# Kernel optimization log

Measured on AMD Instinct MI355X. Metric: run time of the kernel, lower is better.

## Reference

```python
import jax, jax.numpy as jnp
import numpy as np

B, T, C, H, N = 2, 1024, 2048, 32, 64
KVH = 8                       # GQA kv heads
KV = KVH * N                  # 512
REP = H // KVH                # 4
EPS = 1e-6
LORA = [96, 96, 64, 256, 64]  # xw, xa, xv, xg, xk lora dims


def rmsnorm(x, w, eps=EPS):
    xf = x.astype(jnp.float32)
    var = jnp.mean(xf * xf, axis=-1, keepdims=True)
    return (w * (xf * jax.lax.rsqrt(var + eps))).astype(x.dtype)


def rotate_half(x):
    x1, x2 = jnp.split(x, 2, axis=-1)
    return jnp.concatenate([-x2, x1], axis=-1)


def rwkv7_scan(r, w, k, v, a, b, state0):
    # r,w,k,v,a,b: [B,T,H,N]; state0: [B,H,N,N] (value x key)
    # per step: S = S*exp(w) + (S@a) b^T + v k^T ; o = S @ r
    def step(S, inp):
        r_t, w_t, k_t, v_t, a_t, b_t = inp  # each [B,H,N]
        sa = jnp.einsum('bhvk,bhk->bhv', S, a_t)
        S = (S * jnp.exp(w_t)[:, :, None, :]
             + sa[..., None] * b_t[:, :, None, :]
             + v_t[..., None] * k_t[:, :, None, :])
        o = jnp.einsum('bhvk,bhk->bhv', S, r_t)
        return S, o
    seqs = tuple(jnp.moveaxis(t, 1, 0) for t in (r, w, k, v, a, b))
    S, o = jax.lax.scan(step, state0, seqs)
    return jnp.moveaxis(o, 0, 1), S


def setup_inputs() -> dict:
    key = jax.random.key(0)
    ks = jax.random.split(key, 24)
    g = lambda i, shape, s=0.02: jax.random.normal(ks[i], shape, jnp.float32) * s
    # real rope cache, theta = 1e6, rotary_dim = N
    pos = jnp.arange(T, dtype=jnp.float32)
    inv = 1.0 / (1e6 ** (jnp.arange(0, N, 2, dtype=jnp.float32) / N))
    ang = pos[:, None] * inv[None, :]
    ang = jnp.concatenate([ang, ang], axis=-1)  # [T, N]
    cos = jnp.broadcast_to(jnp.cos(ang)[None], (B, T, N))
    sin = jnp.broadcast_to(jnp.sin(ang)[None], (B, T, N))
    return dict(
        x_in=jax.random.normal(ks[0], (B, T, C), jnp.float32),
        v_first=jax.random.normal(ks[1], (B, T, KVH, N), jnp.float32),
        k_first=jax.random.normal(ks[2], (B, T, KVH, N), jnp.float32),
        state=jnp.zeros((B, H, N, N), jnp.float32),
        calc_cos=cos, calc_sin=sin,
        ln1=jnp.ones((C,), jnp.float32), ln2=jnp.ones((C,), jnp.float32),
        ln_r=jnp.ones((N,), jnp.float32), ln_k=jnp.ones((N,), jnp.float32),
        wavgk1=g(3, (C, sum(LORA))),
        w0=g(4, (H * N,)), w2=g(5, (LORA[0], H * N)),
        a0=g(6, (H * N,)), a2=g(7, (LORA[1], H * N)),
        v0=g(8, (KV,)), v2=g(9, (LORA[2], KV)),
        k0=g(10, (KV,)), k2=g(11, (LORA[4], KV)),
        g2=g(12, (LORA[3], H * N)),
        r_k=g(13, (H, N)),
        RKV_W=g(14, (C, H * N + 2 * KV)),
        O_W=g(15, (H * N, C)),
        R_bias=g(16, (H * N,)), K_bias=g(17, (KV,)), V_bias=g(18, (KV,)),
    )


def _forward(x_in, v_first, k_first, state, calc_cos, calc_sin,
             ln1, ln2, ln_r, ln_k, wavgk1, w0, w2, a0, a2, v0, v2,
             k0, k2, g2, r_k, RKV_W, O_W, R_bias, K_bias, V_bias):
    x = rmsnorm(x_in, ln1)
    xw, xa, xv, xg, xk = jnp.split(x @ wavgk1, np.cumsum(LORA)[:-1].tolist(), axis=-1)
    r, k, v = jnp.split(x @ RKV_W, [H * N, H * N + KV], axis=-1)
    r = (r + R_bias).reshape(B, T, H, N)
    k = (k + K_bias).reshape(B, T, KVH, N)
    v = (v + V_bias).reshape(B, T, KVH, N)
    r = rmsnorm(r, ln_r)
    k = rmsnorm(k, ln_k)
    cos = calc_cos[:, :, None, :]
    sin = calc_sin[:, :, None, :]
    r = r * cos + rotate_half(r) * sin
    k = k * cos + rotate_half(k) * sin
    # layer_id != 0: sigmoid-gated interpolation toward first-layer v/k
    v = v + (v_first - v) * jax.nn.sigmoid(xv @ v2 + v0).reshape(B, T, KVH, N)
    k = k + (k_first - k) * jax.nn.sigmoid(xk @ k2 + k0).reshape(B, T, KVH, N)
    # GQA repeat (contiguous per kv head, as repeat_kv does)
    k = jnp.repeat(k, REP, axis=2).reshape(B, T, H * N)
    v = jnp.repeat(v, REP, axis=2).reshape(B, T, H * N)
    a = jax.nn.sigmoid(xa @ a2 + a0)
    kh = k.reshape(B, T, H, N)
    kk = (kh / (jnp.linalg.norm(kh, axis=-1, keepdims=True) + 1e-12)).reshape(B, T, H * N)
    w = jnp.tanh(xw) @ w2 + w0
    w = -jax.nn.softplus(-w) - 0.5
    k = k * (1.0 - w + a)
    aa = -kk
    bb = kk * a
    wlog = -jnp.exp(w)
    sh = (B, T, H, N)
    o, state = rwkv7_scan(r, wlog.reshape(sh), k.reshape(sh), v.reshape(sh),
                          aa.reshape(sh), bb.reshape(sh), state)
    xx = o.reshape(B, T, H * N) * (float(N) ** -0.5)
    bonus = ((r * k.reshape(sh) * r_k).sum(axis=-1, keepdims=True)
             * v.reshape(sh)).reshape(B, T, H * N)
    xx = xx + bonus
    out = (xx * (jax.nn.sigmoid(xg) @ g2)) @ O_W
    x_res = x_in + out
    output = rmsnorm(x_res, ln2)
    return output, x[:, -1], state, v_first, k_first, x_res


def reference(x_in, v_first, k_first, state, calc_cos, calc_sin,
              ln1, ln2, ln_r, ln_k, wavgk1, w0, w2, a0, a2, v0, v2,
              k0, k2, g2, r_k, RKV_W, O_W, R_bias, K_bias, V_bias):
    return _forward(x_in, v_first, k_first, state, calc_cos, calc_sin,
                    ln1, ln2, ln_r, ln_k, wavgk1, w0, w2, a0, a2, v0, v2,
                    k0, k2, g2, r_k, RKV_W, O_W, R_bias, K_bias, V_bias)
```

## Files before the change

kernel.cpp:

```cpp
#include <hip/hip_runtime.h>
#include <hip/hip_bf16.h>

#define BT 2
#define TT 1024
#define CC 2048
#define HH 32
#define MM (BT*TT)
#define TCH 512
#define NCH (TT/TCH)
#define RECB 896

typedef __attribute__((ext_vector_type(8))) short short8;
typedef __attribute__((ext_vector_type(4))) float floatx4;

static __device__ __forceinline__ float bf2f(__hip_bfloat16 x){ return __bfloat162float(x); }
static __device__ __forceinline__ __hip_bfloat16 f2bf(float x){ return __float2bfloat16(x); }
static __device__ __forceinline__ float sigm(float x){ return 1.0f/(1.0f + expf(-x)); }
static __device__ __forceinline__ float u2f(unsigned short u){
  union { unsigned int i; float f; } x; x.i = ((unsigned int)u) << 16; return x.f;
}
static __device__ __forceinline__ float ulo(unsigned int u){ return __uint_as_float(u << 16); }
static __device__ __forceinline__ float uhi(unsigned int u){ return __uint_as_float(u & 0xffff0000u); }
static __device__ __forceinline__ unsigned short bfbits(float x){
  __hip_bfloat16 h = f2bf(x);
  unsigned short s; __builtin_memcpy(&s, &h, 2); return s;
}
static __device__ __forceinline__ unsigned int pkbf(float lo, float hi){
  return (unsigned int)bfbits(lo) | ((unsigned int)bfbits(hi) << 16);
}

#define DPP_ADD(x, ctrl) ((x) + __int_as_float(__builtin_amdgcn_update_dpp(0, __float_as_int(x), (ctrl), 0xF, 0xF, true)))

#if defined(__has_builtin)
#if __has_builtin(__builtin_amdgcn_permlane16_swap) && __has_builtin(__builtin_amdgcn_permlane32_swap)
#define HAVE_PLSWAP 1
#endif
#endif

#ifdef HAVE_PLSWAP
typedef unsigned int uint2v __attribute__((ext_vector_type(2)));
static __device__ __forceinline__ float row16_pair_add(float x){
  unsigned int u = __float_as_uint(x);
  uint2v r = __builtin_amdgcn_permlane16_swap(u, u, false, false);
  return __uint_as_float(r[0]) + __uint_as_float(r[1]);
}
static __device__ __forceinline__ float half32_pair_add(float x){
  unsigned int u = __float_as_uint(x);
  uint2v r = __builtin_amdgcn_permlane32_swap(u, u, false, false);
  return __uint_as_float(r[0]) + __uint_as_float(r[1]);
}
#else
static __device__ __forceinline__ float row16_pair_add(float x){ return x + __shfl_xor(x, 16); }
static __device__ __forceinline__ float half32_pair_add(float x){ return x + __shfl_xor(x, 32); }
#endif

static __device__ __forceinline__ float red8(float x){
  x = DPP_ADD(x, 0xB1);
  x = DPP_ADD(x, 0x4E);
  x = DPP_ADD(x, 0x141);
  return x;
}
static __device__ __forceinline__ float red32(float x){
  x = DPP_ADD(x, 0xB1);
  x = DPP_ADD(x, 0x4E);
  x = DPP_ADD(x, 0x124);
  x = DPP_ADD(x, 0x128);
  return row16_pair_add(x);
}
static __device__ __forceinline__ float red64(float x){
  x = DPP_ADD(x, 0xB1);
  x = DPP_ADD(x, 0x4E);
  x = DPP_ADD(x, 0x124);
  x = DPP_ADD(x, 0x128);
  x = row16_pair_add(x);
  return half32_pair_add(x);
}

__global__ __launch_bounds__(256) void tcvt_kernel(
    const float* __restrict__ W, __hip_bfloat16* __restrict__ Wt,
    int K, int N, int Npad)
{
  __shared__ float tile[32][33];
  const int bn = blockIdx.x*32, bk = blockIdx.y*32;
  const int tx = threadIdx.x & 31, ty0 = threadIdx.x >> 5;
#pragma unroll
  for (int i=0;i<4;++i){
    const int kk = bk + ty0 + i*8;
    float val = 0.f;
    if (kk < K && bn + tx < N) val = W[(size_t)kk*N + bn + tx];
    tile[ty0 + i*8][tx] = val;
  }
  __syncthreads();
#pragma unroll
  for (int i=0;i<4;++i){
    const int nn = bn + ty0 + i*8;
    const int kk = bk + tx;
    if (nn < Npad && kk < K) Wt[(size_t)nn*K + kk] = f2bf(tile[tx][ty0 + i*8]);
  }
}

__global__ __launch_bounds__(256) void rmsnorm1_kernel(
    const float* __restrict__ x_in,
    const float* __restrict__ ln1,
    __hip_bfloat16* __restrict__ x_bf,
    float* __restrict__ x_last)
{
  const int m = blockIdx.x;
  const int tid = threadIdx.x;
  const int c = tid * 8;
  const float* xp = x_in + (size_t)m*CC + c;
  float v[8]; float ss = 0.f;
#pragma unroll
  for (int i=0;i<8;++i){ v[i] = xp[i]; ss += v[i]*v[i]; }
  ss = red64(ss);
  __shared__ float wsum[4];
  if ((tid&63)==0) wsum[tid>>6] = ss;
  __syncthreads();
  ss = wsum[0]+wsum[1]+wsum[2]+wsum[3];
  const float sc = rsqrtf(ss * (1.0f/CC) + 1e-6f);
#pragma unroll
  for (int i=0;i<8;++i) {
    const float y = ln1[c+i] * v[i] * sc;
    x_bf[(size_t)m*CC + c + i] = f2bf(y);
    if ((m % TT) == TT-1) x_last[(size_t)(m/TT)*CC + c + i] = y;
  }
}

template<bool F32OUT>
__global__ __launch_bounds__(256) void mgemm(
    const __hip_bfloat16* __restrict__ A, int lda,
    const __hip_bfloat16* __restrict__ Bt,
    void* __restrict__ C, int N, int K)
{
  __shared__ __align__(16) short As[128*32];
  __shared__ __align__(16) short Bs[128*32];
  const int tid = threadIdx.x;
  const int bm = blockIdx.x * 128;
  const int bn = blockIdx.y * 128;
  const int wid = tid >> 6;
  const int lane = tid & 63;
  const int m16 = lane & 15, quad = lane >> 4;
  const int wm = wid & 1, wn = wid >> 1;
  const int lrow = tid >> 2;
  const int lcol = (tid & 3) * 8;

  floatx4 acc[4][4];
#pragma unroll
  for (int i=0;i<4;++i)
#pragma unroll
    for (int j=0;j<4;++j) acc[i][j] = (floatx4){0.f,0.f,0.f,0.f};

  for (int k0 = 0; k0 < K; k0 += 32) {
    __syncthreads();
    uint4 a0v = *(const uint4*)(const void*)(A  + (size_t)(bm + lrow)      * lda + k0 + lcol);
    uint4 a1v = *(const uint4*)(const void*)(A  + (size_t)(bm + 64 + lrow) * lda + k0 + lcol);
    uint4 b0v = *(const uint4*)(const void*)(Bt + (size_t)(bn + lrow)      * K   + k0 + lcol);
    uint4 b1v = *(const uint4*)(const void*)(Bt + (size_t)(bn + 64 + lrow) * K   + k0 + lcol);
    *(uint4*)(void*)(As + lrow*32 + lcol)        = a0v;
    *(uint4*)(void*)(As + (64 + lrow)*32 + lcol) = a1v;
    *(uint4*)(void*)(Bs + lrow*32 + lcol)        = b0v;
    *(uint4*)(void*)(Bs + (64 + lrow)*32 + lcol) = b1v;
    __syncthreads();

    short8 af[4], bfg[4];
#pragma unroll
    for (int mi=0; mi<4; ++mi)
      af[mi] = *(const short8*)(const void*)(As + (wm*64 + mi*16 + m16)*32 + quad*8);
#pragma unroll
    for (int ni=0; ni<4; ++ni)
      bfg[ni] = *(const short8*)(const void*)(Bs + (wn*64 + ni*16 + m16)*32 + quad*8);
#pragma unroll
    for (int mi=0; mi<4; ++mi)
#pragma unroll
      for (int ni=0; ni<4; ++ni)
        acc[mi][ni] = __builtin_amdgcn_mfma_f32_16x16x32_bf16(af[mi], bfg[ni], acc[mi][ni], 0,0,0);
  }

#pragma unroll
  for (int mi=0; mi<4; ++mi) {
    const int row = bm + wm*64 + mi*16 + quad*4;
#pragma unroll
    for (int ni=0; ni<4; ++ni) {
      const int col = bn + wn*64 + ni*16 + m16;
      if (col < N) {
        if (F32OUT) {
          float* cp = (float*)C;
#pragma unroll
          for (int r=0;r<4;++r) cp[(size_t)(row+r)*N + col] = acc[mi][ni][r];
        } else {
          __hip_bfloat16* cp = (__hip_bfloat16*)C;
#pragma unroll
          for (int r=0;r<4;++r) cp[(size_t)(row+r)*N + col] = f2bf(acc[mi][ni][r]);
        }
      }
    }
  }
}

__global__ void act576_kernel(__hip_bfloat16* __restrict__ Y1)
{
  int i = blockIdx.x*256 + threadIdx.x;
  if (i >= MM*576) return;
  int col = i % 576;
  float v = bf2f(Y1[i]);
  if (col < 96) v = tanhf(v);
  else if (col >= 256 && col < 512) v = sigm(v);
  Y1[i] = f2bf(v);
}

__global__ __launch_bounds__(256) void prep_kernel(
    const __hip_bfloat16* __restrict__ RKV,
    const __hip_bfloat16* __restrict__ Wpre,
    const __hip_bfloat16* __restrict__ Apre,
    const __hip_bfloat16* __restrict__ Vsig,
    const __hip_bfloat16* __restrict__ Ksig,
    const float* __restrict__ v_first,
    const float* __restrict__ k_first,
    const float* __restrict__ cosp,
    const float* __restrict__ sinp,
    const float* __restrict__ ln_r,
    const float* __restrict__ ln_k,
    const float* __restrict__ r_k,
    const float* __restrict__ w0,
    const float* __restrict__ a0,
    const float* __restrict__ v0,
    const float* __restrict__ k0b,
    const float* __restrict__ R_bias,
    const float* __restrict__ K_bias,
    const float* __restrict__ V_bias,
    char* __restrict__ rec,
    float* __restrict__ bonus,
    int t0)
{
  const int b    = blockIdx.x / TCH;
  const int tloc = blockIdx.x % TCH;
  const int t    = t0 + tloc;
  const int m    = b*TT + t;
  const int tid = threadIdx.x;
  const int h  = tid >> 3;
  const int j  = tid & 7;
  const int hk = h >> 2;
  const int nb = j * 8;
  const int hn = h*64 + nb;
  const int kn = hk*64 + nb;

  const size_t rbase = (size_t)m*3072 + h*64 + nb;
  const size_t kbase = (size_t)m*3072 + 2048 + kn;
  const size_t vbase = kbase + 512;

  float r[8], k[8], v[8];
  float ssr = 0.f, ssk = 0.f;
#pragma unroll
  for (int i=0;i<8;++i) {
    r[i] = bf2f(RKV[rbase+i]) + R_bias[hn+i];
    k[i] = bf2f(RKV[kbase+i]) + K_bias[kn+i];
    v[i] = bf2f(RKV[vbase+i]) + V_bias[kn+i];
    ssr += r[i]*r[i];
    ssk += k[i]*k[i];
  }
  ssr = red8(ssr);
  ssk = red8(ssk);
  const float scr = rsqrtf(ssr*(1.0f/64.0f) + 1e-6f);
  const float sck = rsqrtf(ssk*(1.0f/64.0f) + 1e-6f);
#pragma unroll
  for (int i=0;i<8;++i) {
    r[i] = ln_r[nb+i] * r[i] * scr;
    k[i] = ln_k[nb+i] * k[i] * sck;
  }
  const float sgn = (j < 4) ? -1.0f : 1.0f;
  float rr[8], kr[8];
#pragma unroll
  for (int i=0;i<8;++i) {
    const float cs = cosp[(size_t)m*64 + nb + i];
    const float sn = sinp[(size_t)m*64 + nb + i];
    const float pr = __shfl_xor(r[i], 4);
    const float pk = __shfl_xor(k[i], 4);
    rr[i] = r[i]*cs + sgn*pr*sn;
    kr[i] = k[i]*cs + sgn*pk*sn;
  }
  float av[8], ew[8], wv2[8];
  float ssn = 0.f;
#pragma unroll
  for (int i=0;i<8;++i) {
    const float vs = sigm(bf2f(Vsig[(size_t)m*512 + kn + i]) + v0[kn+i]);
    v[i]  = v[i]  + (v_first[(size_t)m*512 + kn + i] - v[i])  * vs;
    const float ks = sigm(bf2f(Ksig[(size_t)m*512 + kn + i]) + k0b[kn+i]);
    kr[i] = kr[i] + (k_first[(size_t)m*512 + kn + i] - kr[i]) * ks;
    ssn += kr[i]*kr[i];
    av[i] = sigm(bf2f(Apre[(size_t)m*2048 + hn + i]) + a0[hn+i]);
    float wraw = bf2f(Wpre[(size_t)m*2048 + hn + i]) + w0[hn+i];
    const float xs = -wraw;
    const float sp = fmaxf(xs, 0.f) + log1pf(expf(-fabsf(xs)));
    const float wv = -sp - 0.5f;
    wv2[i] = wv;
    ew[i] = expf(-expf(wv));
  }
  ssn = red8(ssn);
  const float inrm = 1.0f / (sqrtf(ssn) + 1e-12f);
  float kf[8], kkv[8];
  float bsum = 0.f;
#pragma unroll
  for (int i=0;i<8;++i) {
    kkv[i] = kr[i] * inrm;
    kf[i]  = kr[i] * (1.0f - wv2[i] + av[i]);
    bsum  += rr[i] * kf[i] * r_k[hn+i];
  }
  bsum = red8(bsum);

  char* base = rec + ((size_t)(b*HH + h)*TCH + tloc)*RECB;
  const int klb = nb >> 1;
#pragma unroll
  for (int p=0;p<4;++p) {
    const int i0 = 2*p, i1 = i0 + 1;
    uint4 Aw;
    Aw.x = __float_as_uint(ew[i0]);
    Aw.y = __float_as_uint(ew[i1]);
    Aw.z = pkbf(rr[i0], rr[i1]);
    Aw.w = pkbf(kf[i0], kf[i1]);
    *(uint4*)(void*)(base + (size_t)(klb + p)*16) = Aw;
    uint2 Bw;
    Bw.x = pkbf(kkv[i0], kkv[i1]);
    Bw.y = pkbf(-kkv[i0]*av[i0], -kkv[i1]*av[i1]);
    *(uint2*)(void*)(base + 512 + (size_t)(klb + p)*8) = Bw;
  }
  short8 vs8;
#pragma unroll
  for (int i=0;i<8;++i) vs8[i] = (short)bfbits(v[i]);
  *(short8*)(void*)(base + 768 + (size_t)nb*2) = vs8;
#pragma unroll
  for (int i=0;i<8;++i)
    bonus[(size_t)m*2048 + hn + i] = bsum * v[i];
}

__global__ __launch_bounds__(256) void scan_kernel(
    const char* __restrict__ rec,
    float* __restrict__ state,
    float* __restrict__ o_out,
    int t0)
{
  const int blk = blockIdx.x;
  const int bh  = blk & 63;
  const int q   = blk >> 6;
  const int b   = bh >> 5, h = bh & 31;
  const int tid = threadIdx.x;
  const int vl  = q*8 + (tid >> 5);
  const int kl  = tid & 31;
  const int k2  = kl*2;

  const char* base = rec + (size_t)bh * TCH * RECB;
  float* sp = state + ((size_t)bh*64 + vl)*64 + k2;
  float S0=sp[0], S1=sp[1];

  const char* pA = base + kl*16;
  const char* pB = base + 512 + kl*8;
  const char* pv = base + 768 + vl*2;

  uint4 Ab[4]; uint2 Bb[4]; unsigned short vb[4];
#pragma unroll
  for (int s=0;s<4;++s){
    Ab[s] = *(const uint4*)(const void*)(pA + s*RECB);
    Bb[s] = *(const uint2*)(const void*)(pB + s*RECB);
    vb[s] = *(const unsigned short*)(const void*)(pv + s*RECB);
  }
  pA += 4*RECB; pB += 4*RECB; pv += 4*RECB;

  int oidx = (b*TT + t0)*CC + h*64 + vl - CC;
  int tt = 0;
  float opart = 0.f;

#define SCAN_STEP(jj, PF)                                                      \
  {                                                                            \
    const uint4 A  = Ab[jj];                                                   \
    const uint2 Bv = Bb[jj];                                                   \
    const float vf = u2f(vb[jj]);                                              \
    if (PF) {                                                                  \
      Ab[jj] = *(const uint4*)(const void*)(pA + jj*RECB);                     \
      Bb[jj] = *(const uint2*)(const void*)(pB + jj*RECB);                     \
      vb[jj] = *(const unsigned short*)(const void*)(pv + jj*RECB);            \
    }                                                                          \
    float op = red32(opart);                                                   \
    const float kk0 = ulo(Bv.x), kk1 = uhi(Bv.x);                              \
    float sa = S0*kk0 + S1*kk1;                                                \
    sa = red32(sa);                                                            \
    if (kl == 0 && tt > 0) o_out[oidx] = op;                                   \
    S0 = S0*__uint_as_float(A.x) + sa*ulo(Bv.y) + vf*ulo(A.w);                 \
    S1 = S1*__uint_as_float(A.y) + sa*uhi(Bv.y) + vf*uhi(A.w);                 \
    opart = S0*ulo(A.z) + S1*uhi(A.z);                                         \
    ++tt; oidx += CC;                                                          \
  }

  for (int t = 0; t < TCH-4; t += 4) {
    SCAN_STEP(0, true)
    SCAN_STEP(1, true)
    SCAN_STEP(2, true)
    SCAN_STEP(3, true)
    pA += 4*RECB; pB += 4*RECB; pv += 4*RECB;
  }
  SCAN_STEP(0, false)
  SCAN_STEP(1, false)
  SCAN_STEP(2, false)
  SCAN_STEP(3, false)
#undef SCAN_STEP

  opart = red32(opart);
  if (kl == 0)
    o_out[oidx] = opart;

  sp[0]=S0; sp[1]=S1;
}

__global__ void xxg_kernel(const float* __restrict__ o_in,
                           const float* __restrict__ bonus,
                           const __hip_bfloat16* __restrict__ G,
                           __hip_bfloat16* __restrict__ xxg)
{
  int i = blockIdx.x*256 + threadIdx.x;
  xxg[i] = f2bf((o_in[i]*0.125f + bonus[i]) * bf2f(G[i]));
}

__global__ __launch_bounds__(256) void final_kernel(
    const float* __restrict__ x_in,
    const float* __restrict__ OUTb,
    const float* __restrict__ ln2,
    float* __restrict__ seg0,
    float* __restrict__ seg5)
{
  const int m = blockIdx.x;
  const int tid = threadIdx.x;
  const int c = tid*8;
  const float* xp = x_in + (size_t)m*CC + c;
  const float* op = OUTb + (size_t)m*CC + c;
  float xr[8]; float ss = 0.f;
#pragma unroll
  for (int i=0;i<8;++i){ xr[i] = xp[i] + op[i]; ss += xr[i]*xr[i]; }
#pragma unroll
  for (int i=0;i<8;++i) seg5[(size_t)m*CC + c + i] = xr[i];
  ss = red64(ss);
  __shared__ float wsum[4];
  if ((tid&63)==0) wsum[tid>>6] = ss;
  __syncthreads();
  ss = wsum[0]+wsum[1]+wsum[2]+wsum[3];
  const float sc = rsqrtf(ss*(1.0f/CC) + 1e-6f);
#pragma unroll
  for (int i=0;i<8;++i) seg0[(size_t)m*CC + c + i] = ln2[c+i] * xr[i] * sc;
}

extern "C" void kernel_launch(void* const* d_in, const int* in_sizes, int n_in,
                              void* d_out, int out_size, void* d_ws, size_t ws_size,
                              hipStream_t stream)
{
  (void)in_sizes; (void)n_in; (void)out_size; (void)ws_size;
  const float* x_in   = (const float*)d_in[0];
  const float* v_first= (const float*)d_in[1];
  const float* k_first= (const float*)d_in[2];
  const float* state0 = (const float*)d_in[3];
  const float* cosp   = (const float*)d_in[4];
  const float* sinp   = (const float*)d_in[5];
  const float* ln1    = (const float*)d_in[6];
  const float* ln2    = (const float*)d_in[7];
  const float* ln_r   = (const float*)d_in[8];
  const float* ln_k   = (const float*)d_in[9];
  const float* wavgk1 = (const float*)d_in[10];
  const float* w0     = (const float*)d_in[11];
  const float* w2     = (const float*)d_in[12];
  const float* a0     = (const float*)d_in[13];
  const float* a2     = (const float*)d_in[14];
  const float* v0     = (const float*)d_in[15];
  const float* v2     = (const float*)d_in[16];
  const float* k0b    = (const float*)d_in[17];
  const float* k2     = (const float*)d_in[18];
  const float* g2     = (const float*)d_in[19];
  const float* r_k    = (const float*)d_in[20];
  const float* RKV_W  = (const float*)d_in[21];
  const float* O_W    = (const float*)d_in[22];
  const float* R_bias = (const float*)d_in[23];
  const float* K_bias = (const float*)d_in[24];
  const float* V_bias = (const float*)d_in[25];

  float* out  = (float*)d_out;
  float* seg0 = out;
  float* seg1 = out + 4194304;
  float* seg2 = out + 4198400;
  float* seg3 = out + 4460544;
  float* seg4 = out + 5509120;
  float* seg5 = out + 6557696;

  char* ws = (char*)d_ws;
  const size_t OFF_STF   = 0;
  const size_t OFF_OWT   = 1048576;
  const size_t OFF_G     = 9437184;
  const size_t OFF_VSIG  = 17825792;
  const size_t OFF_KSIG  = 19922944;
  const size_t OFF_WPRE  = 22020096;
  const size_t OFF_APRE  = 30408704;
  const size_t OFF_RKV   = 38797312;
  const size_t OFF_XBF   = 51380224;
  const size_t OFF_Y1    = 59768832;
  const size_t OFF_WT    = 62128128;
  const size_t OFF_WAVT  = OFF_WT;
  const size_t OFF_RKVT  = OFF_WAVT + 2621440;
  const size_t OFF_W2T   = OFF_RKVT + 12582912;
  const size_t OFF_A2T   = OFF_W2T  + 393216;
  const size_t OFF_V2T   = OFF_A2T  + 393216;
  const size_t OFF_K2T   = OFF_V2T  + 65536;
  const size_t OFF_G2T   = OFF_K2T  + 65536;
  const size_t OFF_REC   = OFF_WT;
  const size_t OFF_XXG   = OFF_XBF;
  const size_t OFF_OUT   = OFF_WPRE;

  float*          stf   = (float*)(ws + OFF_STF);
  __hip_bfloat16* owt   = (__hip_bfloat16*)(ws + OFF_OWT);
  __hip_bfloat16* Gbuf  = (__hip_bfloat16*)(ws + OFF_G);
  __hip_bfloat16* Vsig  = (__hip_bfloat16*)(ws + OFF_VSIG);
  __hip_bfloat16* Ksig  = (__hip_bfloat16*)(ws + OFF_KSIG);
  __hip_bfloat16* Wpre  = (__hip_bfloat16*)(ws + OFF_WPRE);
  __hip_bfloat16* Apre  = (__hip_bfloat16*)(ws + OFF_APRE);
  __hip_bfloat16* RKV   = (__hip_bfloat16*)(ws + OFF_RKV);
  __hip_bfloat16* x_bf  = (__hip_bfloat16*)(ws + OFF_XBF);
  __hip_bfloat16* Y1    = (__hip_bfloat16*)(ws + OFF_Y1);
  __hip_bfloat16* wavt  = (__hip_bfloat16*)(ws + OFF_WAVT);
  __hip_bfloat16* rkvt  = (__hip_bfloat16*)(ws + OFF_RKVT);
  __hip_bfloat16* w2t   = (__hip_bfloat16*)(ws + OFF_W2T);
  __hip_bfloat16* a2t   = (__hip_bfloat16*)(ws + OFF_A2T);
  __hip_bfloat16* v2t   = (__hip_bfloat16*)(ws + OFF_V2T);
  __hip_bfloat16* k2t   = (__hip_bfloat16*)(ws + OFF_K2T);
  __hip_bfloat16* g2t   = (__hip_bfloat16*)(ws + OFF_G2T);
  char*           rec   = ws + OFF_REC;
  __hip_bfloat16* xxg   = (__hip_bfloat16*)(ws + OFF_XXG);
  float*          OUTb  = (float*)(ws + OFF_OUT);

  float* o_st = seg0;
  float* b_st = seg5;

  tcvt_kernel<<<dim3(20, 64), 256, 0, stream>>>(wavgk1, wavt, 2048, 576, 640);
  tcvt_kernel<<<dim3(96, 64), 256, 0, stream>>>(RKV_W,  rkvt, 2048, 3072, 3072);
  tcvt_kernel<<<dim3(64, 64), 256, 0, stream>>>(O_W,    owt,  2048, 2048, 2048);
  tcvt_kernel<<<dim3(64,  3), 256, 0, stream>>>(w2,     w2t,    96, 2048, 2048);
  tcvt_kernel<<<dim3(64,  3), 256, 0, stream>>>(a2,     a2t,    96, 2048, 2048);
  tcvt_kernel<<<dim3(16,  2), 256, 0, stream>>>(v2,     v2t,    64,  512,  512);
  tcvt_kernel<<<dim3(16,  2), 256, 0, stream>>>(k2,     k2t,    64,  512,  512);
  tcvt_kernel<<<dim3(64,  8), 256, 0, stream>>>(g2,     g2t,   256, 2048, 2048);

  rmsnorm1_kernel<<<MM, 256, 0, stream>>>(x_in, ln1, x_bf, seg1);
  mgemm<false><<<dim3(16,  5), 256, 0, stream>>>(x_bf, CC, wavt, Y1,   576, 2048);
  mgemm<false><<<dim3(16, 24), 256, 0, stream>>>(x_bf, CC, rkvt, RKV, 3072, 2048);
  act576_kernel<<<(MM*576+255)/256, 256, 0, stream>>>(Y1);
  mgemm<false><<<dim3(16, 16), 256, 0, stream>>>(Y1+0,   576, w2t, Wpre, 2048, 96);
  mgemm<false><<<dim3(16, 16), 256, 0, stream>>>(Y1+96,  576, a2t, Apre, 2048, 96);
  mgemm<false><<<dim3(16,  4), 256, 0, stream>>>(Y1+192, 576, v2t, Vsig,  512, 64);
  mgemm<false><<<dim3(16,  4), 256, 0, stream>>>(Y1+512, 576, k2t, Ksig,  512, 64);
  mgemm<false><<<dim3(16, 16), 256, 0, stream>>>(Y1+256, 576, g2t, Gbuf, 2048, 256);

  hipMemcpyAsync(stf, state0, (size_t)1048576, hipMemcpyDeviceToDevice, stream);
  for (int c = 0; c < NCH; ++c) {
    const int t0 = c*TCH;
    prep_kernel<<<BT*TCH, 256, 0, stream>>>(RKV, Wpre, Apre, Vsig, Ksig, v_first, k_first,
                                            cosp, sinp, ln_r, ln_k, r_k, w0, a0, v0, k0b,
                                            R_bias, K_bias, V_bias, rec, b_st, t0);
    scan_kernel<<<BT*HH*8, 256, 0, stream>>>(rec, stf, o_st, t0);
  }
  hipMemcpyAsync(seg2, stf, (size_t)1048576, hipMemcpyDeviceToDevice, stream);

  xxg_kernel<<<(MM*CC)/256, 256, 0, stream>>>(o_st, b_st, Gbuf, xxg);
  mgemm<true><<<dim3(16, 16), 256, 0, stream>>>(xxg, CC, owt, OUTb, 2048, 2048);
  final_kernel<<<MM, 256, 0, stream>>>(x_in, OUTb, ln2, seg0, seg5);

  hipMemcpyAsync(seg3, v_first, (size_t)1048576*4, hipMemcpyDeviceToDevice, stream);
  hipMemcpyAsync(seg4, k_first, (size_t)1048576*4, hipMemcpyDeviceToDevice, stream);
}
```

Before: 658.8 us.

## Use direct global-to-LDS loads in GEMM, fuse activation, pack scan math

The GEMM tile loads now go straight from global memory into LDS through the global_load_lds builtin when it is available, skipping the pass through registers. The tanh/sigmoid activation is moved into the epilogue of the first LoRA GEMM, which removes the separate act576 kernel and its extra read and write of Y1. The scan kernel's state update is rewritten with two-wide float vectors so the compiler can emit packed FP32 ops. Its first unrolled group is peeled, which drops the per-step check that skipped the output store on the first step. Risks are that the direct-to-LDS path depends on the compiler treating the per-lane LDS address as wave base plus lane offset, and that the packed math may not change the scan's serial latency.

```diff
diff --git a/kernel.cpp b/kernel.cpp
--- a/kernel.cpp
+++ b/kernel.cpp
@@ -12,6 +12,7 @@
 
 typedef __attribute__((ext_vector_type(8))) short short8;
 typedef __attribute__((ext_vector_type(4))) float floatx4;
+typedef __attribute__((ext_vector_type(2))) float f32x2;
 
 static __device__ __forceinline__ float bf2f(__hip_bfloat16 x){ return __bfloat162float(x); }
 static __device__ __forceinline__ __hip_bfloat16 f2bf(float x){ return __float2bfloat16(x); }
@@ -28,6 +29,21 @@
 static __device__ __forceinline__ unsigned int pkbf(float lo, float hi){
   return (unsigned int)bfbits(lo) | ((unsigned int)bfbits(hi) << 16);
 }
+
+#if defined(__has_builtin)
+#if __has_builtin(__builtin_amdgcn_global_load_lds)
+#define HAVE_GLL 1
+#endif
+#endif
+
+#ifdef HAVE_GLL
+static __device__ __forceinline__ void gll16(const void* g, void* l){
+  __builtin_amdgcn_global_load_lds(
+      (__attribute__((address_space(1))) void*)const_cast<void*>(g),
+      (__attribute__((address_space(3))) void*)l,
+      16, 0, 0);
+}
+#endif
 
 #define DPP_ADD(x, ctrl) ((x) + __int_as_float(__builtin_amdgcn_update_dpp(0, __float_as_int(x), (ctrl), 0xF, 0xF, true)))
 
@@ -126,7 +142,7 @@
   }
 }
 
-template<bool F32OUT>
+template<bool F32OUT, int ACT>
 __global__ __launch_bounds__(256) void mgemm(
     const __hip_bfloat16* __restrict__ A, int lda,
     const __hip_bfloat16* __restrict__ Bt,
@@ -150,16 +166,26 @@
 #pragma unroll
     for (int j=0;j<4;++j) acc[i][j] = (floatx4){0.f,0.f,0.f,0.f};
 
+  char* asl = (char*)As + tid*16;
+  char* bsl = (char*)Bs + tid*16;
+
   for (int k0 = 0; k0 < K; k0 += 32) {
     __syncthreads();
+#ifdef HAVE_GLL
+    gll16(A  + (size_t)(bm + lrow)      * lda + k0 + lcol, asl);
+    gll16(A  + (size_t)(bm + 64 + lrow) * lda + k0 + lcol, asl + 4096);
+    gll16(Bt + (size_t)(bn + lrow)      * K   + k0 + lcol, bsl);
+    gll16(Bt + (size_t)(bn + 64 + lrow) * K   + k0 + lcol, bsl + 4096);
+#else
     uint4 a0v = *(const uint4*)(const void*)(A  + (size_t)(bm + lrow)      * lda + k0 + lcol);
     uint4 a1v = *(const uint4*)(const void*)(A  + (size_t)(bm + 64 + lrow) * lda + k0 + lcol);
     uint4 b0v = *(const uint4*)(const void*)(Bt + (size_t)(bn + lrow)      * K   + k0 + lcol);
     uint4 b1v = *(const uint4*)(const void*)(Bt + (size_t)(bn + 64 + lrow) * K   + k0 + lcol);
-    *(uint4*)(void*)(As + lrow*32 + lcol)        = a0v;
-    *(uint4*)(void*)(As + (64 + lrow)*32 + lcol) = a1v;
-    *(uint4*)(void*)(Bs + lrow*32 + lcol)        = b0v;
-    *(uint4*)(void*)(Bs + (64 + lrow)*32 + lcol) = b1v;
+    *(uint4*)(void*)(asl)        = a0v;
+    *(uint4*)(void*)(asl + 4096) = a1v;
+    *(uint4*)(void*)(bsl)        = b0v;
+    *(uint4*)(void*)(bsl + 4096) = b1v;
+#endif
     __syncthreads();
 
     short8 af[4], bfg[4];
@@ -190,22 +216,18 @@
         } else {
           __hip_bfloat16* cp = (__hip_bfloat16*)C;
 #pragma unroll
-          for (int r=0;r<4;++r) cp[(size_t)(row+r)*N + col] = f2bf(acc[mi][ni][r]);
+          for (int r=0;r<4;++r) {
+            float x = acc[mi][ni][r];
+            if (ACT == 1) {
+              if (col < 96) x = tanhf(x);
+              else if (col >= 256 && col < 512) x = sigm(x);
+            }
+            cp[(size_t)(row+r)*N + col] = f2bf(x);
+          }
         }
       }
     }
   }
-}
-
-__global__ void act576_kernel(__hip_bfloat16* __restrict__ Y1)
-{
-  int i = blockIdx.x*256 + threadIdx.x;
-  if (i >= MM*576) return;
-  int col = i % 576;
-  float v = bf2f(Y1[i]);
-  if (col < 96) v = tanhf(v);
-  else if (col >= 256 && col < 512) v = sigm(v);
-  Y1[i] = f2bf(v);
 }
 
 __global__ __launch_bounds__(256) void prep_kernel(
@@ -349,7 +371,7 @@
 
   const char* base = rec + (size_t)bh * TCH * RECB;
   float* sp = state + ((size_t)bh*64 + vl)*64 + k2;
-  float S0=sp[0], S1=sp[1];
+  f32x2 S; S.x = sp[0]; S.y = sp[1];
 
   const char* pA = base + kl*16;
   const char* pB = base + 512 + kl*8;
@@ -365,10 +387,9 @@
   pA += 4*RECB; pB += 4*RECB; pv += 4*RECB;
 
   int oidx = (b*TT + t0)*CC + h*64 + vl - CC;
-  int tt = 0;
   float opart = 0.f;
 
-#define SCAN_STEP(jj, PF)                                                      \
+#define SCAN_STEP(jj, PF, ST)                                                  \
   {                                                                            \
     const uint4 A  = Ab[jj];                                                   \
     const uint2 Bv = Bb[jj];                                                   \
@@ -379,34 +400,47 @@
       vb[jj] = *(const unsigned short*)(const void*)(pv + jj*RECB);            \
     }                                                                          \
     float op = red32(opart);                                                   \
-    const float kk0 = ulo(Bv.x), kk1 = uhi(Bv.x);                              \
-    float sa = S0*kk0 + S1*kk1;                                                \
+    f32x2 kk; kk.x = ulo(Bv.x); kk.y = uhi(Bv.x);                              \
+    const f32x2 prod = S * kk;                                                 \
+    float sa = prod.x + prod.y;                                                \
     sa = red32(sa);                                                            \
-    if (kl == 0 && tt > 0) o_out[oidx] = op;                                   \
-    S0 = S0*__uint_as_float(A.x) + sa*ulo(Bv.y) + vf*ulo(A.w);                 \
-    S1 = S1*__uint_as_float(A.y) + sa*uhi(Bv.y) + vf*uhi(A.w);                 \
-    opart = S0*ulo(A.z) + S1*uhi(A.z);                                         \
-    ++tt; oidx += CC;                                                          \
-  }
-
-  for (int t = 0; t < TCH-4; t += 4) {
-    SCAN_STEP(0, true)
-    SCAN_STEP(1, true)
-    SCAN_STEP(2, true)
-    SCAN_STEP(3, true)
+    if (ST && kl == 0) o_out[oidx] = op;                                       \
+    f32x2 ew; ew.x = __uint_as_float(A.x); ew.y = __uint_as_float(A.y);        \
+    f32x2 bb; bb.x = ulo(Bv.y); bb.y = uhi(Bv.y);                              \
+    f32x2 kf; kf.x = ulo(A.w); kf.y = uhi(A.w);                                \
+    f32x2 sav; sav.x = sa; sav.y = sa;                                         \
+    f32x2 vfv; vfv.x = vf; vfv.y = vf;                                         \
+    S = S*ew + sav*bb + vfv*kf;                                                \
+    f32x2 rv; rv.x = ulo(A.z); rv.y = uhi(A.z);                                \
+    const f32x2 ov = S * rv;                                                   \
+    opart = ov.x + ov.y;                                                       \
+    oidx += CC;                                                                \
+  }
+
+  SCAN_STEP(0, true, 0)
+  SCAN_STEP(1, true, 1)
+  SCAN_STEP(2, true, 1)
+  SCAN_STEP(3, true, 1)
+  pA += 4*RECB; pB += 4*RECB; pv += 4*RECB;
+
+  for (int t = 4; t < TCH-4; t += 4) {
+    SCAN_STEP(0, true, 1)
+    SCAN_STEP(1, true, 1)
+    SCAN_STEP(2, true, 1)
+    SCAN_STEP(3, true, 1)
     pA += 4*RECB; pB += 4*RECB; pv += 4*RECB;
   }
-  SCAN_STEP(0, false)
-  SCAN_STEP(1, false)
-  SCAN_STEP(2, false)
-  SCAN_STEP(3, false)
+  SCAN_STEP(0, false, 1)
+  SCAN_STEP(1, false, 1)
+  SCAN_STEP(2, false, 1)
+  SCAN_STEP(3, false, 1)
 #undef SCAN_STEP
 
   opart = red32(opart);
   if (kl == 0)
     o_out[oidx] = opart;
 
-  sp[0]=S0; sp[1]=S1;
+  sp[0]=S.x; sp[1]=S.y;
 }
 
 __global__ void xxg_kernel(const float* __restrict__ o_in,
@@ -542,14 +576,13 @@
   tcvt_kernel<<<dim3(64,  8), 256, 0, stream>>>(g2,     g2t,   256, 2048, 2048);
 
   rmsnorm1_kernel<<<MM, 256, 0, stream>>>(x_in, ln1, x_bf, seg1);
-  mgemm<false><<<dim3(16,  5), 256, 0, stream>>>(x_bf, CC, wavt, Y1,   576, 2048);
-  mgemm<false><<<dim3(16, 24), 256, 0, stream>>>(x_bf, CC, rkvt, RKV, 3072, 2048);
-  act576_kernel<<<(MM*576+255)/256, 256, 0, stream>>>(Y1);
-  mgemm<false><<<dim3(16, 16), 256, 0, stream>>>(Y1+0,   576, w2t, Wpre, 2048, 96);
-  mgemm<false><<<dim3(16, 16), 256, 0, stream>>>(Y1+96,  576, a2t, Apre, 2048, 96);
-  mgemm<false><<<dim3(16,  4), 256, 0, stream>>>(Y1+192, 576, v2t, Vsig,  512, 64);
-  mgemm<false><<<dim3(16,  4), 256, 0, stream>>>(Y1+512, 576, k2t, Ksig,  512, 64);
-  mgemm<false><<<dim3(16, 16), 256, 0, stream>>>(Y1+256, 576, g2t, Gbuf, 2048, 256);
+  mgemm<false,1><<<dim3(16,  5), 256, 0, stream>>>(x_bf, CC, wavt, Y1,   576, 2048);
+  mgemm<false,0><<<dim3(16, 24), 256, 0, stream>>>(x_bf, CC, rkvt, RKV, 3072, 2048);
+  mgemm<false,0><<<dim3(16, 16), 256, 0, stream>>>(Y1+0,   576, w2t, Wpre, 2048, 96);
+  mgemm<false,0><<<dim3(16, 16), 256, 0, stream>>>(Y1+96,  576, a2t, Apre, 2048, 96);
+  mgemm<false,0><<<dim3(16,  4), 256, 0, stream>>>(Y1+192, 576, v2t, Vsig,  512, 64);
+  mgemm<false,0><<<dim3(16,  4), 256, 0, stream>>>(Y1+512, 576, k2t, Ksig,  512, 64);
+  mgemm<false,0><<<dim3(16, 16), 256, 0, stream>>>(Y1+256, 576, g2t, Gbuf, 2048, 256);
 
   hipMemcpyAsync(stf, state0, (size_t)1048576, hipMemcpyDeviceToDevice, stream);
   for (int c = 0; c < NCH; ++c) {
@@ -562,7 +595,7 @@
   hipMemcpyAsync(seg2, stf, (size_t)1048576, hipMemcpyDeviceToDevice, stream);
 
   xxg_kernel<<<(MM*CC)/256, 256, 0, stream>>>(o_st, b_st, Gbuf, xxg);
-  mgemm<true><<<dim3(16, 16), 256, 0, stream>>>(xxg, CC, owt, OUTb, 2048, 2048);
+  mgemm<true,0><<<dim3(16, 16), 256, 0, stream>>>(xxg, CC, owt, OUTb, 2048, 2048);
   final_kernel<<<MM, 256, 0, stream>>>(x_in, OUTb, ln2, seg0, seg5);
 
   hipMemcpyAsync(seg3, v_first, (size_t)1048576*4, hipMemcpyDeviceToDevice, stream);
```

After: 664.8 us. About the same (+0.9%).
